# Kernel tuning notes

Hardware: AMD Instinct MI355X
Metric: run time of the kernel (lower is better)

## Reference

```python
import jax, jax.numpy as jnp
import numpy as np

T = 16                       # sample_duration
FG_THRESH, BG_HI, BG_LO = 0.5, 0.5, 0.1
ROIS_PER_IMAGE, FG_PER_IMAGE = 128, 32   # conf.TRAIN.BATCH_SIZE, round(0.25*128)
STDS = jnp.tile(jnp.array([0.1, 0.1, 0.2, 0.2], jnp.float32), T)  # BBOX_NORMALIZE_STDS tiled; means are 0


def _tube_iou(rois, gts):
    # rois [b,M,T,4], gts [b,K,T,4] -> mean per-frame IoU over non-empty frames [b,M,K]
    r = rois[:, :, None]             # [b,M,1,T,4]
    g = gts[:, None]                 # [b,1,K,T,4]
    iw = jnp.clip(jnp.minimum(r[..., 2], g[..., 2]) - jnp.maximum(r[..., 0], g[..., 0]) + 1.0, 0.0)
    ih = jnp.clip(jnp.minimum(r[..., 3], g[..., 3]) - jnp.maximum(r[..., 1], g[..., 1]) + 1.0, 0.0)
    inter = iw * ih
    ar = (r[..., 2] - r[..., 0] + 1.0) * (r[..., 3] - r[..., 1] + 1.0)
    ag = (g[..., 2] - g[..., 0] + 1.0) * (g[..., 3] - g[..., 1] + 1.0)
    r_empty = jnp.all(r == 0.0, -1)
    g_empty = jnp.all(g == 0.0, -1)
    iou = jnp.where(r_empty | g_empty, 0.0, inter / (ar + ag - inter))
    valid = ~(r_empty & g_empty)
    return iou.sum(-1) / jnp.maximum(valid.sum(-1), 1).astype(iou.dtype)


def _bbox_transform(ex, gt):
    ew = ex[..., 2] - ex[..., 0] + 1.0
    eh = ex[..., 3] - ex[..., 1] + 1.0
    ecx = ex[..., 0] + 0.5 * ew
    ecy = ex[..., 1] + 0.5 * eh
    gw = gt[..., 2] - gt[..., 0] + 1.0
    gh = gt[..., 3] - gt[..., 1] + 1.0
    gcx = gt[..., 0] + 0.5 * gw
    gcy = gt[..., 1] + 0.5 * gh
    return jnp.stack([(gcx - ecx) / ew, (gcy - ecy) / eh,
                      jnp.log(gw / ew), jnp.log(gh / eh)], axis=-1)


def _sample_one(ov, lab, key):
    # ov, lab: [M]; jit-safe fg/bg sampling matching the torch control flow
    M = ov.shape[0]
    k1, k2, k3, k4 = jax.random.split(key, 4)
    fg = ov >= FG_THRESH
    bg = (ov < BG_HI) & (ov >= BG_LO)
    fg_num = fg.sum()
    bg_num = bg.sum()
    # random permutation with fg (resp. bg) indices first
    order_fg = jnp.argsort(jnp.where(fg, jax.random.uniform(k1, (M,)), 2.0))
    order_bg = jnp.argsort(jnp.where(bg, jax.random.uniform(k2, (M,)), 2.0))
    fg_this = jnp.where(bg_num > 0, jnp.minimum(FG_PER_IMAGE, fg_num),
                        jnp.where(fg_num > 0, ROIS_PER_IMAGE, 0))
    r = jnp.arange(ROIS_PER_IMAGE)
    fg_repl = order_fg[(jax.random.uniform(k3, (ROIS_PER_IMAGE,)) * jnp.maximum(fg_num, 1)).astype(jnp.int32)]
    fg_idx = jnp.where(bg_num > 0, order_fg[r], fg_repl)  # no-replacement when bg exists, else with replacement
    bg_idx = order_bg[(jax.random.uniform(k4, (ROIS_PER_IMAGE,)) * jnp.maximum(bg_num, 1)).astype(jnp.int32)]
    is_fg = r < fg_this
    keep = jnp.where(is_fg, fg_idx, bg_idx)
    return keep, jnp.where(is_fg, lab[keep], 0.0)


def _forward(all_tubes, gt_boxes, gt_tubes_all):
    b, N, _ = all_tubes.shape
    A = gt_boxes.shape[1]
    # gt tube coords + label of first nonzero-labelled frame
    gt_tubes = gt_boxes[..., :4].reshape(b, A, T * 4)
    fr_lab = gt_boxes[..., 4]                                    # [b,A,T]
    has = jnp.any(fr_lab != 0, axis=2)
    first = jnp.argmax(fr_lab != 0, axis=2)
    labels_gt = jnp.where(has, jnp.take_along_axis(fr_lab, first[..., None], 2)[..., 0], 0.0)
    # scatter tube coords into frames [round(start), round(end)] (vectorized mask-scatter)
    sf = jnp.round(all_tubes[..., 3]).astype(jnp.int32)[..., None]
    ef = jnp.round(all_tubes[..., 6]).astype(jnp.int32)[..., None]
    f = jnp.arange(T)[None, None]
    fmask = ((f >= sf) & (f <= ef)).astype(all_tubes.dtype)      # [b,N,T]
    coords = all_tubes[..., jnp.array([1, 2, 4, 5])]             # [b,N,4]
    all_rois = fmask[..., None] * coords[:, :, None, :]          # [b,N,T,4]
    off = jnp.broadcast_to(jnp.arange(b, dtype=all_rois.dtype)[:, None, None], (b, N, 1))
    all_rois = jnp.concatenate([off, all_rois.reshape(b, N, T * 4)], axis=2)
    # append gt boxes/tubes as extra proposals (batch col = 0)
    gt_app = jnp.concatenate([jnp.zeros((b, A, 1), all_rois.dtype), gt_tubes], axis=2)
    all_rois = jnp.concatenate([all_rois, gt_app], axis=1)       # [b,N+A,1+4T]
    gt_tubes_app = jnp.concatenate([jnp.zeros((b, A, 1), all_tubes.dtype), gt_tubes_all[..., :-1]], axis=2)
    all_tubes_c = jnp.concatenate([all_tubes, gt_tubes_app], axis=1)  # [b,N+A,7]
    # IoU overlaps + gt assignment
    ov = _tube_iou(all_rois[..., 1:].reshape(b, N + A, T, 4),
                   gt_tubes.reshape(b, A, T, 4))                 # [b,N+A,A]
    max_ov = ov.max(axis=2)
    gt_asg = ov.argmax(axis=2)
    labels = jnp.take_along_axis(labels_gt, gt_asg, axis=1)      # [b,N+A]
    # fg/bg sampling (fixed key -> deterministic)
    keys = jax.random.split(jax.random.key(42), b)
    keep, labels_b = jax.vmap(_sample_one)(max_ov, labels, keys)  # [b,R]
    rois_b = jnp.take_along_axis(all_rois, keep[..., None], axis=1)
    rois_b = rois_b.at[..., 0].set(jnp.arange(b, dtype=rois_b.dtype)[:, None])
    tubes_b = jnp.take_along_axis(all_tubes_c, keep[..., None], axis=1)
    tubes_b = tubes_b.at[..., 0].set(jnp.arange(b, dtype=tubes_b.dtype)[:, None])
    asg_k = jnp.take_along_axis(gt_asg, keep, axis=1)
    gt_rois_b = jnp.take_along_axis(gt_tubes, asg_k[..., None], axis=1)  # [b,R,4T]
    tgt = _bbox_transform(rois_b[..., 1:].reshape(b, ROIS_PER_IMAGE, T, 4),
                          gt_rois_b.reshape(b, ROIS_PER_IMAGE, T, 4)).reshape(b, ROIS_PER_IMAGE, T * 4)
    tgt = tgt / STDS
    pos = (labels_b > 0)[..., None]
    bbox_targets = jnp.where(pos, tgt, 0.0)
    inside = jnp.where(pos, jnp.ones_like(tgt), 0.0)
    outside = (inside > 0).astype(tgt.dtype)
    return rois_b, tubes_b, labels_b, bbox_targets, inside, outside


def setup_inputs() -> dict:
    key = jax.random.key(0)
    ks = jax.random.split(key, 9)
    b, N, A = 8, 20000, 5
    x1 = jax.random.uniform(ks[0], (b, N), minval=0.0, maxval=200.0)
    y1 = jax.random.uniform(ks[1], (b, N), minval=0.0, maxval=200.0)
    x2 = x1 + jax.random.uniform(ks[2], (b, N), minval=8.0, maxval=120.0)
    y2 = y1 + jax.random.uniform(ks[3], (b, N), minval=8.0, maxval=120.0)
    sf = jax.random.randint(ks[4], (b, N), 0, T).astype(jnp.float32)
    ef = jnp.minimum(sf + jax.random.randint(ks[5], (b, N), 0, T).astype(jnp.float32), T - 1.0)
    bidx = jnp.broadcast_to(jnp.arange(b, dtype=jnp.float32)[:, None], (b, N))
    all_tubes = jnp.stack([bidx, x1, y1, sf, x2, y2, ef], axis=-1)
    gx1 = jax.random.uniform(ks[6], (b, A, T), minval=0.0, maxval=200.0)
    gy1 = jax.random.uniform(ks[7], (b, A, T), minval=0.0, maxval=200.0)
    gx2 = gx1 + 60.0
    gy2 = gy1 + 60.0
    glab = jax.random.randint(ks[8], (b, A), 1, 21).astype(jnp.float32)[..., None]
    gt_boxes = jnp.stack([gx1, gy1, gx2, gy2, jnp.broadcast_to(glab, (b, A, T))], axis=-1)
    gt_tubes_all = jnp.concatenate([
        jnp.zeros((b, A, 1)), gx1.min(-1, keepdims=True), gy1.min(-1, keepdims=True),
        jnp.zeros((b, A, 1)), gx2.max(-1, keepdims=True), gy2.max(-1, keepdims=True),
        jnp.full((b, A, 1), T - 1.0)], axis=-1).astype(jnp.float32)
    return {"all_tubes": all_tubes, "gt_boxes": gt_boxes, "gt_tubes_all": gt_tubes_all}


def reference(all_tubes, gt_boxes, gt_tubes_all):
    return _forward(all_tubes, gt_boxes, gt_tubes_all)
```

## Files before the change

kernel.cpp:

```cpp
#include <hip/hip_runtime.h>
#include <stdint.h>

#define T 16
#define NB 8
#define NROI 20000
#define NA 5
#define MM (NROI + NA)
#define MMPAD 20224
#define RPI 128
#define FGPI 32
#define NBLK 79
#define NBLK2 20
#define SORTCAP 32768
#define LCAP 16384
#define NBUCK 2048

__host__ __device__ __forceinline__ void tf2x32(uint32_t k0, uint32_t k1,
                                                uint32_t x0, uint32_t x1,
                                                uint32_t& o0, uint32_t& o1) {
  uint32_t ks2 = k0 ^ k1 ^ 0x1BD11BDAu;
  x0 += k0; x1 += k1;
#define ROUND(r) { x0 += x1; x1 = (x1 << (r)) | (x1 >> (32 - (r))); x1 ^= x0; }
  ROUND(13) ROUND(15) ROUND(26) ROUND(6)
  x0 += k1; x1 += ks2 + 1u;
  ROUND(17) ROUND(29) ROUND(16) ROUND(24)
  x0 += ks2; x1 += k0 + 2u;
  ROUND(13) ROUND(15) ROUND(26) ROUND(6)
  x0 += k0; x1 += k1 + 3u;
  ROUND(17) ROUND(29) ROUND(16) ROUND(24)
  x0 += k1; x1 += ks2 + 4u;
  ROUND(13) ROUND(15) ROUND(26) ROUND(6)
  x0 += ks2; x1 += k0 + 5u;
#undef ROUND
  o0 = x0; o1 = x1;
}

__device__ __forceinline__ uint32_t rbits32(uint32_t k0, uint32_t k1, uint32_t i) {
  uint32_t a, b; tf2x32(k0, k1, 0u, i, a, b); return a ^ b;
}
__device__ __forceinline__ float uni01(uint32_t bits) {
  return __uint_as_float((bits >> 9) | 0x3f800000u) - 1.0f;
}

struct Keys { uint32_t k[NB][4][2]; };

__global__ __launch_bounds__(256) void k_iou(const float* __restrict__ tubes,
                                             const float* __restrict__ gtb,
                                             unsigned long long* __restrict__ pk) {
  int img = blockIdx.y;
  int a = blockIdx.z;
  int b = blockIdx.x;
  int tid = threadIdx.x;
  int n = b * 256 + tid;
  bool valid = n < MM;
  int nn = valid ? n : MM - 1;
  bool isroi = nn < NROI;

  __shared__ float tub[256 * 7];
  __shared__ float4 g4[NA][T];
  __shared__ float gar[NA][T];
  {
    int rcnt = min(256, NROI - b * 256);
    int f4cnt = (rcnt * 7) >> 2;
    const float4* src = (const float4*)(tubes + (size_t)img * NROI * 7 + (size_t)b * 256 * 7);
    float4* dst = (float4*)tub;
    for (int i = tid; i < f4cnt; i += 256) dst[i] = src[i];
  }
  for (int i = tid; i < NA * T; i += 256) {
    int aa = i / T, t = i - aa * T;
    const float* p = gtb + (((size_t)img * NA + aa) * T + t) * 5;
    float4 v = make_float4(p[0], p[1], p[2], p[3]);
    g4[aa][t] = v;
    gar[aa][t] = (v.z - v.x + 1.0f) * (v.w - v.y + 1.0f);
  }
  __syncthreads();

  float s = 0.0f;
  if (isroi) {
    const float* p = &tub[tid * 7];
    float rx1 = p[1], ry1 = p[2], rx2 = p[4], ry2 = p[5];
    int sf = (int)rintf(p[3]), ef = (int)rintf(p[6]);
    float rar = (rx2 - rx1 + 1.0f) * (ry2 - ry1 + 1.0f);
#pragma unroll
    for (int t = 0; t < T; ++t) {
      float4 gg = g4[a][t]; float ag = gar[a][t];
      float iw = fmaxf(fminf(rx2, gg.z) - fmaxf(rx1, gg.x) + 1.0f, 0.0f);
      float ih = fmaxf(fminf(ry2, gg.w) - fmaxf(ry1, gg.y) + 1.0f, 0.0f);
      float inter = iw * ih;
      float q = inter / (rar + ag - inter);
      s += ((t >= sf) && (t <= ef)) ? q : 0.0f;
    }
  } else {
    int ga = nn - NROI;
#pragma unroll
    for (int t = 0; t < T; ++t) {
      float4 e = g4[ga][t]; float ar = gar[ga][t];
      float4 gg = g4[a][t]; float ag = gar[a][t];
      float iw = fmaxf(fminf(e.z, gg.z) - fmaxf(e.x, gg.x) + 1.0f, 0.0f);
      float ih = fmaxf(fminf(e.w, gg.w) - fmaxf(e.y, gg.y) + 1.0f, 0.0f);
      float inter = iw * ih;
      s += inter / (ar + ag - inter);
    }
  }
  if (valid) {
    float ovv = s / 16.0f;
    unsigned long long pkv = ((unsigned long long)__float_as_uint(ovv) << 3)
                           | (unsigned long long)(7 - a);
    atomicMax(&pk[(size_t)img * MMPAD + n], pkv);
  }
}

__global__ __launch_bounds__(1024) void k_classify(const unsigned long long* __restrict__ pk,
                                                   uint64_t* __restrict__ slots,
                                                   int* __restrict__ cnts2,
                                                   int* __restrict__ mins2,
                                                   Keys keys) {
  int img = blockIdx.y;
  int b = blockIdx.x;
  int tid = threadIdx.x;
  int n = b * 1024 + tid;
  bool valid = n < MM;
  int nn = valid ? n : MM - 1;
  int lane = tid & 63;
  int w = tid >> 6;

  unsigned long long p = pk[(size_t)img * MMPAD + nn];
  float best = __uint_as_float((uint32_t)(p >> 3));

  bool isfg = valid && (best >= 0.5f);
  bool isbg = valid && (best < 0.5f) && (best >= 0.1f);

  __shared__ int wcnt[16][2];
  __shared__ int wmn[16][2];
  unsigned long long mfg = __ballot(isfg);
  unsigned long long mbg = __ballot(isbg);
  unsigned long long mnf = __ballot(valid && !isfg);
  unsigned long long mnb = __ballot(valid && !isbg);
  int wavebase = b * 1024 + w * 64;
  if (lane == 0) {
    wcnt[w][0] = __popcll(mfg);
    wcnt[w][1] = __popcll(mbg);
    wmn[w][0] = mnf ? (wavebase + __ffsll(mnf) - 1) : 0x7FFFFFFF;
    wmn[w][1] = mnb ? (wavebase + __ffsll(mnb) - 1) : 0x7FFFFFFF;
  }
  __syncthreads();

  if (tid == 0) {
    int tf = 0, tb = 0, mf = 0x7FFFFFFF, mb = 0x7FFFFFFF;
#pragma unroll
    for (int w2 = 0; w2 < 16; ++w2) {
      tf += wcnt[w2][0]; tb += wcnt[w2][1];
      mf = min(mf, wmn[w2][0]); mb = min(mb, wmn[w2][1]);
    }
    int idx = img * NBLK2 + b;
    cnts2[idx]                = tf;
    cnts2[NB * NBLK2 + idx]   = tb;
    mins2[idx]                = mf;
    mins2[NB * NBLK2 + idx]   = mb;
  }

  int pf = 0, pb = 0;
  for (int w2 = 0; w2 < w; ++w2) { pf += wcnt[w2][0]; pb += wcnt[w2][1]; }
  unsigned long long below = (1ULL << lane) - 1ULL;
  uint64_t* slotF = slots + (size_t)(img * 2 + 0) * SORTCAP + b * 1024;
  uint64_t* slotB = slots + (size_t)(img * 2 + 1) * SORTCAP + b * 1024;
  if (isfg) {
    int pos = pf + __popcll(mfg & below);
    uint32_t m = rbits32(keys.k[img][0][0], keys.k[img][0][1], (uint32_t)n) >> 9;
    slotF[pos] = ((uint64_t)m << 32) | (uint32_t)n;
  }
  if (isbg) {
    int pos = pb + __popcll(mbg & below);
    uint32_t m = rbits32(keys.k[img][1][0], keys.k[img][1][1], (uint32_t)n) >> 9;
    slotB[pos] = ((uint64_t)m << 32) | (uint32_t)n;
  }
}

__global__ __launch_bounds__(1024) void k_sortsample(const float* __restrict__ tubes,
                                                     const float* __restrict__ gtb,
                                                     const float* __restrict__ gta,
                                                     const unsigned long long* __restrict__ pk,
                                                     uint64_t* __restrict__ slots,
                                                     const int* __restrict__ cnts2,
                                                     const int* __restrict__ mins2,
                                                     Keys keys,
                                                     float* __restrict__ out) {
  __shared__ uint64_t buf[LCAP];
  __shared__ int hist[NBUCK];
  __shared__ int pref[NBUCK + 1];
  __shared__ int wsum[16];
  __shared__ int scnt[NBLK2], spref[NBLK2 + 1];
  __shared__ int s_tot, s_oth, s_mn;
  __shared__ int s_keep[RPI];
  __shared__ int s_ak[RPI];
  __shared__ float s_lab[RPI];
  __shared__ unsigned char s_own[RPI];

  int list = blockIdx.x;
  int img = list >> 1;
  int which = list & 1;
  int tid = threadIdx.x;
  int lane = tid & 63, wv = tid >> 6;
  uint64_t* arr = slots + (size_t)(img * 2 + which) * SORTCAP;
  const int* cn = cnts2 + which * NB * NBLK2 + img * NBLK2;
  const int* co = cnts2 + (1 - which) * NB * NBLK2 + img * NBLK2;
  const int* mn = mins2 + which * NB * NBLK2 + img * NBLK2;

  if (tid < NBLK2) scnt[tid] = cn[tid];
  for (int i = tid; i < NBUCK; i += 1024) hist[i] = 0;
  __syncthreads();
  if (tid == 0) {
    int acc = 0, mmn = 0x7FFFFFFF, oth = 0;
#pragma unroll
    for (int bb = 0; bb < NBLK2; ++bb) {
      spref[bb] = acc; acc += scnt[bb];
      mmn = min(mmn, mn[bb]); oth += co[bb];
    }
    spref[NBLK2] = acc; s_tot = acc; s_mn = mmn; s_oth = oth;
  }
  __syncthreads();
  int cnt = s_tot, min_non = s_mn;
  int fg_num = (which == 0) ? cnt : s_oth;
  int bg_num = (which == 0) ? s_oth : cnt;
  bool ldsPath = (cnt <= LCAP);

  if (cnt > 0 && ldsPath) {
    for (int s = tid; s < NBLK2 * 1024; s += 1024) {
      int bb = s >> 10, i = s & 1023;
      if (i < scnt[bb]) {
        uint64_t key = arr[s];
        atomicAdd(&hist[(int)(key >> 44)], 1);
      }
    }
    __syncthreads();
    {
      int a0 = hist[2 * tid], a1 = hist[2 * tid + 1];
      int ps = a0 + a1;
      int v = ps;
      for (int off = 1; off < 64; off <<= 1) {
        int u = __shfl_up(v, off);
        if (lane >= off) v += u;
      }
      if (lane == 63) wsum[wv] = v;
      __syncthreads();
      if (tid == 0) {
        int acc = 0;
        for (int i = 0; i < 16; ++i) { int x = wsum[i]; wsum[i] = acc; acc += x; }
        pref[NBUCK] = acc;
      }
      __syncthreads();
      int excl = v - ps + wsum[wv];
      pref[2 * tid] = excl;
      pref[2 * tid + 1] = excl + a0;
      hist[2 * tid] = excl;
      hist[2 * tid + 1] = excl + a0;
    }
    __syncthreads();
    for (int s = tid; s < NBLK2 * 1024; s += 1024) {
      int bb = s >> 10, i = s & 1023;
      if (i < scnt[bb]) {
        uint64_t key = arr[s];
        int pos = atomicAdd(&hist[(int)(key >> 44)], 1);
        buf[pos] = key;
      }
    }
    __syncthreads();
  } else if (cnt > 1) {
    for (int bb = 0; bb < NBLK2; ++bb) {
      uint64_t v = 0; int c = scnt[bb];
      if (tid < c) v = arr[bb * 1024 + tid];
      __syncthreads();
      if (tid < c) arr[spref[bb] + tid] = v;
      __syncthreads();
    }
    int n2 = 2; while (n2 < cnt) n2 <<= 1;
    for (int i = cnt + tid; i < n2; i += 1024) arr[i] = ~0ULL;
    __syncthreads();
    for (int k = 2; k <= n2; k <<= 1) {
      for (int j = k >> 1; j; j >>= 1) {
        for (int i = tid; i < n2; i += 1024) {
          int ixj = i ^ j;
          if (ixj > i) {
            uint64_t a = arr[i], bv = arr[ixj];
            bool up = (i & k) == 0;
            if (up ? (a > bv) : (a < bv)) { arr[i] = bv; arr[ixj] = a; }
          }
        }
        __syncthreads();
      }
    }
    __syncthreads();
  }

  float* o_rois = out;
  float* o_tub = out + (size_t)NB * RPI * 65;
  float* o_lab = o_tub + (size_t)NB * RPI * 7;
  float* o_tgt = o_lab + (size_t)NB * RPI;
  float* o_in  = o_tgt + (size_t)NB * RPI * 64;
  float* o_ou  = o_in  + (size_t)NB * RPI * 64;

  int fg_this = (bg_num > 0) ? min(FGPI, fg_num) : (fg_num > 0 ? RPI : 0);

#define RANKQ(L, OUTV) {                                               \
    int l_ = (L);                                                      \
    if (ldsPath) {                                                     \
      int lo_ = 0, hi_ = NBUCK;                                        \
      while (hi_ - lo_ > 1) {                                          \
        int mid_ = (lo_ + hi_) >> 1;                                   \
        if (pref[mid_] <= l_) lo_ = mid_; else hi_ = mid_;             \
      }                                                                \
      int base_ = pref[lo_], cnt_ = pref[lo_ + 1] - base_;             \
      int ll_ = l_ - base_;                                            \
      uint64_t ans_ = 0;                                               \
      for (int i_ = 0; i_ < cnt_; ++i_) {                              \
        uint64_t ki_ = buf[base_ + i_];                                \
        int cl_ = 0;                                                   \
        for (int j_ = 0; j_ < cnt_; ++j_) cl_ += (buf[base_ + j_] < ki_); \
        if (cl_ == ll_) { ans_ = ki_; break; }                         \
      }                                                                \
      OUTV = (int)(uint32_t)(ans_ & 0xffffffffULL);                    \
    } else {                                                           \
      OUTV = (int)(uint32_t)(arr[l_] & 0xffffffffULL);                 \
    }                                                                  \
  }

  if (tid < RPI) {
    int r = tid;
    bool is_fg = r < fg_this;
    bool own = (is_fg == (which == 0));
    s_own[r] = own ? 1 : 0;
    if (own) {
      int keep;
      if (which == 0) {
        if (bg_num > 0) {
          RANKQ(r, keep)
        } else {
          float u3 = uni01(rbits32(keys.k[img][2][0], keys.k[img][2][1], (uint32_t)r));
          int q = (int)(u3 * (float)max(fg_num, 1));
          if (q >= fg_num) {
            if (fg_num >= MM) { RANKQ(MM - 1, keep) } else keep = min_non;
          } else {
            RANKQ(q, keep)
          }
        }
      } else {
        float u4 = uni01(rbits32(keys.k[img][3][0], keys.k[img][3][1], (uint32_t)r));
        int qb = (int)(u4 * (float)max(bg_num, 1));
        if (qb >= bg_num) {
          if (bg_num >= MM) { RANKQ(MM - 1, keep) } else keep = min_non;
        } else {
          RANKQ(qb, keep)
        }
      }

      unsigned long long pkv = pk[(size_t)img * MMPAD + keep];
      int ak = 7 - (int)(pkv & 7ULL);
      float glab = gtb[(((size_t)img * NA + ak) * T + 0) * 5 + 4];
      float lab = is_fg ? glab : 0.0f;
      s_keep[r] = keep; s_ak[r] = ak; s_lab[r] = lab;

      size_t row = (size_t)img * RPI + r;
      float* pt = o_tub + row * 7;
      o_rois[row * 65] = (float)img;
      pt[0] = (float)img;
      if (keep < NROI) {
        const float* p = tubes + ((size_t)img * NROI + keep) * 7;
#pragma unroll
        for (int cc = 1; cc < 7; ++cc) pt[cc] = p[cc];
      } else {
        const float* p = gta + ((size_t)img * NA + (keep - NROI)) * 7;
#pragma unroll
        for (int cc = 1; cc < 7; ++cc) pt[cc] = p[cc - 1];
      }
      o_lab[row] = lab;
    }
  }
#undef RANKQ
  __syncthreads();

  for (int i = tid; i < RPI * T; i += 1024) {
    int rl = i >> 4;
    if (!s_own[rl]) continue;
    int t = i & 15;
    size_t row = (size_t)img * RPI + rl;
    int keep = s_keep[rl];
    int ak = s_ak[rl];
    float lab = s_lab[rl];
    bool pos = lab > 0.0f;
    float posf = pos ? 1.0f : 0.0f;

    float ex1, ey1, ex2, ey2;
    if (keep < NROI) {
      const float* p = tubes + ((size_t)img * NROI + keep) * 7;
      int sf = (int)rintf(p[3]), ef = (int)rintf(p[6]);
      bool in = (t >= sf) && (t <= ef);
      ex1 = in ? p[1] : 0.0f; ey1 = in ? p[2] : 0.0f;
      ex2 = in ? p[4] : 0.0f; ey2 = in ? p[5] : 0.0f;
    } else {
      const float* p = gtb + (((size_t)img * NA + (keep - NROI)) * T + t) * 5;
      ex1 = p[0]; ey1 = p[1]; ex2 = p[2]; ey2 = p[3];
    }

    float* pr = o_rois + row * 65 + 1 + 4 * t;
    pr[0] = ex1; pr[1] = ey1; pr[2] = ex2; pr[3] = ey2;

    const float* gp = gtb + (((size_t)img * NA + ak) * T + t) * 5;
    float gx1 = gp[0], gy1 = gp[1], gx2 = gp[2], gy2 = gp[3];
    float ew = ex2 - ex1 + 1.0f, eh = ey2 - ey1 + 1.0f;
    float ecx = ex1 + 0.5f * ew, ecy = ey1 + 0.5f * eh;
    float gw = gx2 - gx1 + 1.0f, gh = gy2 - gy1 + 1.0f;
    float gcx = gx1 + 0.5f * gw, gcy = gy1 + 0.5f * gh;
    float t0 = ((gcx - ecx) / ew) / 0.1f;
    float t1 = ((gcy - ecy) / eh) / 0.1f;
    float t2 = logf(gw / ew) / 0.2f;
    float t3 = logf(gh / eh) / 0.2f;

    *(float4*)(o_tgt + row * 64 + 4 * t) =
        make_float4(pos ? t0 : 0.0f, pos ? t1 : 0.0f, pos ? t2 : 0.0f, pos ? t3 : 0.0f);
    float4 pf4 = make_float4(posf, posf, posf, posf);
    *(float4*)(o_in + row * 64 + 4 * t) = pf4;
    *(float4*)(o_ou + row * 64 + 4 * t) = pf4;
  }
}

extern "C" void kernel_launch(void* const* d_in, const int* in_sizes, int n_in,
                              void* d_out, int out_size, void* d_ws, size_t ws_size,
                              hipStream_t stream) {
  const float* tubes = (const float*)d_in[0];
  const float* gtb   = (const float*)d_in[1];
  const float* gta   = (const float*)d_in[2];
  float* out = (float*)d_out;
  char* ws = (char*)d_ws;

  Keys keys;
  for (int img = 0; img < NB; ++img) {
    uint32_t r0, r1; tf2x32(0u, 42u, 0u, (uint32_t)img, r0, r1);
    for (int j = 0; j < 4; ++j) {
      uint32_t a, b; tf2x32(r0, r1, 0u, (uint32_t)j, a, b);
      keys.k[img][j][0] = a; keys.k[img][j][1] = b;
    }
  }

  int* cnts2 = (int*)ws;
  int* mins2 = (int*)(ws + 1280);
  unsigned long long* pk = (unsigned long long*)(ws + 4096);
  uint64_t* slots = (uint64_t*)(ws + 1298432);

  hipMemsetAsync(pk, 0, (size_t)NB * MMPAD * 8, stream);
  dim3 gI(NBLK, NB, NA);
  k_iou<<<gI, 256, 0, stream>>>(tubes, gtb, pk);
  dim3 gC(NBLK2, NB);
  k_classify<<<gC, 1024, 0, stream>>>(pk, slots, cnts2, mins2, keys);
  k_sortsample<<<16, 1024, 0, stream>>>(tubes, gtb, gta, pk, slots, cnts2, mins2, keys, out);
}
```

Measured before the change: 43.15 us.

## Replace atomicMax overlap packing with per-GT overlap buffer and argmax in classify

The IoU kernel now writes each per-GT overlap to its own slot in a [img, GT, MMPAD] float buffer instead of doing a 64-bit atomicMax into a packed overlap/index word. The classify kernel reads the five overlaps, computes max and argmax itself, and stores a byte-sized assignment array that the sampling kernel reads. This removes the memset launch and the global atomics. In exchange it adds more global writes and reads for the five overlap planes. Tie-breaking now picks the first maximum, matching argmax semantics.

Result: faster. 39.20 us (median of 2 runs) (-9.2%).

```diff
diff --git a/kernel.cpp b/kernel.cpp
--- a/kernel.cpp
+++ b/kernel.cpp
@@ -46,7 +46,7 @@
 
 __global__ __launch_bounds__(256) void k_iou(const float* __restrict__ tubes,
                                              const float* __restrict__ gtb,
-                                             unsigned long long* __restrict__ pk) {
+                                             float* __restrict__ ov) {
   int img = blockIdx.y;
   int a = blockIdx.z;
   int b = blockIdx.x;
@@ -102,15 +102,11 @@
       s += inter / (ar + ag - inter);
     }
   }
-  if (valid) {
-    float ovv = s / 16.0f;
-    unsigned long long pkv = ((unsigned long long)__float_as_uint(ovv) << 3)
-                           | (unsigned long long)(7 - a);
-    atomicMax(&pk[(size_t)img * MMPAD + n], pkv);
-  }
-}
-
-__global__ __launch_bounds__(1024) void k_classify(const unsigned long long* __restrict__ pk,
+  if (valid) ov[((size_t)img * NA + a) * MMPAD + n] = s / 16.0f;
+}
+
+__global__ __launch_bounds__(1024) void k_classify(const float* __restrict__ ov,
+                                                   unsigned char* __restrict__ asg,
                                                    uint64_t* __restrict__ slots,
                                                    int* __restrict__ cnts2,
                                                    int* __restrict__ mins2,
@@ -124,8 +120,19 @@
   int lane = tid & 63;
   int w = tid >> 6;
 
-  unsigned long long p = pk[(size_t)img * MMPAD + nn];
-  float best = __uint_as_float((uint32_t)(p >> 3));
+  const float* base_ov = ov + (size_t)img * NA * MMPAD + nn;
+  float o0 = base_ov[0 * MMPAD];
+  float o1 = base_ov[1 * MMPAD];
+  float o2 = base_ov[2 * MMPAD];
+  float o3 = base_ov[3 * MMPAD];
+  float o4 = base_ov[4 * MMPAD];
+  float best = o0; int barg = 0;
+  if (o1 > best) { best = o1; barg = 1; }
+  if (o2 > best) { best = o2; barg = 2; }
+  if (o3 > best) { best = o3; barg = 3; }
+  if (o4 > best) { best = o4; barg = 4; }
+
+  if (valid) asg[(size_t)img * MM + n] = (unsigned char)barg;
 
   bool isfg = valid && (best >= 0.5f);
   bool isbg = valid && (best < 0.5f) && (best >= 0.1f);
@@ -179,7 +186,7 @@
 __global__ __launch_bounds__(1024) void k_sortsample(const float* __restrict__ tubes,
                                                      const float* __restrict__ gtb,
                                                      const float* __restrict__ gta,
-                                                     const unsigned long long* __restrict__ pk,
+                                                     const unsigned char* __restrict__ asg,
                                                      uint64_t* __restrict__ slots,
                                                      const int* __restrict__ cnts2,
                                                      const int* __restrict__ mins2,
@@ -353,8 +360,7 @@
         }
       }
 
-      unsigned long long pkv = pk[(size_t)img * MMPAD + keep];
-      int ak = 7 - (int)(pkv & 7ULL);
+      int ak = asg[(size_t)img * MM + keep];
       float glab = gtb[(((size_t)img * NA + ak) * T + 0) * 5 + 4];
       float lab = is_fg ? glab : 0.0f;
       s_keep[r] = keep; s_ak[r] = ak; s_lab[r] = lab;
@@ -443,13 +449,13 @@
 
   int* cnts2 = (int*)ws;
   int* mins2 = (int*)(ws + 1280);
-  unsigned long long* pk = (unsigned long long*)(ws + 4096);
-  uint64_t* slots = (uint64_t*)(ws + 1298432);
-
-  hipMemsetAsync(pk, 0, (size_t)NB * MMPAD * 8, stream);
+  unsigned char* asg = (unsigned char*)(ws + 2560);
+  uint64_t* slots = (uint64_t*)(ws + 162600);
+  float* ov = (float*)(ws + 4356904);
+
   dim3 gI(NBLK, NB, NA);
-  k_iou<<<gI, 256, 0, stream>>>(tubes, gtb, pk);
+  k_iou<<<gI, 256, 0, stream>>>(tubes, gtb, ov);
   dim3 gC(NBLK2, NB);
-  k_classify<<<gC, 1024, 0, stream>>>(pk, slots, cnts2, mins2, keys);
-  k_sortsample<<<16, 1024, 0, stream>>>(tubes, gtb, gta, pk, slots, cnts2, mins2, keys, out);
-}
+  k_classify<<<gC, 1024, 0, stream>>>(ov, asg, slots, cnts2, mins2, keys);
+  k_sortsample<<<16, 1024, 0, stream>>>(tubes, gtb, gta, asg, slots, cnts2, mins2, keys, out);
+}
```
